# Optimization experiments

Measured on AMD Instinct MI355X. Metric: run time of the kernel, lower is better.

## Reference

```python
import jax, jax.numpy as jnp
import numpy as np

N = 8000      # nodes
E = 64000     # edges
F = 2560      # in_channels
H = 8         # heads
C = 320       # out_channels per head
G = 16        # graphs in batch
SLOPE = 0.2   # GATv2 default negative_slope


def setup_inputs() -> dict:
    key = jax.random.key(0)
    ks = jax.random.split(key, 20)
    inp = {
        'x': jax.random.normal(ks[0], (N, F), jnp.float32),
        'edge_index': jax.random.randint(ks[1], (2, E), 0, N, dtype=jnp.int64),
        'edge_attr': jax.random.normal(ks[2], (E, 1), jnp.float32),
        'batch': jnp.sort(jax.random.randint(ks[3], (N,), 0, G, dtype=jnp.int64)),
    }
    s_in = 1.0 / np.sqrt(F).astype(np.float32)
    s_att = 1.0 / np.sqrt(C).astype(np.float32)
    k = 4
    for layer in (1, 2):
        inp[f'Wl{layer}'] = jax.random.normal(ks[k + 0], (F, H * C), jnp.float32) * s_in
        inp[f'bl{layer}'] = jnp.zeros((H * C,), jnp.float32)
        inp[f'Wr{layer}'] = jax.random.normal(ks[k + 1], (F, H * C), jnp.float32) * s_in
        inp[f'br{layer}'] = jnp.zeros((H * C,), jnp.float32)
        inp[f'We{layer}'] = jax.random.normal(ks[k + 2], (1, H * C), jnp.float32)
        inp[f'att{layer}'] = jax.random.normal(ks[k + 3], (H, C), jnp.float32) * s_att
        inp[f'bias{layer}'] = jnp.zeros((H * C,), jnp.float32)
        k += 4
    return inp


def gatv2_layer(x, src, dst, edge_attr, Wl, bl, Wr, br, We, att, bias):
    # x: [N,F] -> out: [N, H*C]
    xl = (x @ Wl + bl).reshape(N, H, C)   # source transform (aggregated)
    xr = (x @ Wr + br).reshape(N, H, C)   # target transform
    ee = (edge_attr @ We).reshape(E, H, C)
    m = jax.nn.leaky_relu(xl[src] + xr[dst] + ee, SLOPE)  # [E,H,C]
    score = jnp.einsum('ehc,hc->eh', m, att)               # [E,H]
    # segment softmax over incoming edges of each target node
    smax = jax.ops.segment_max(score, dst, num_segments=N)  # [N,H]
    ex = jnp.exp(score - smax[dst])
    denom = jax.ops.segment_sum(ex, dst, num_segments=N)    # [N,H]
    alpha = ex / denom[dst]                                  # [E,H]
    out = jax.ops.segment_sum(xl[src] * alpha[:, :, None], dst, num_segments=N)
    return out.reshape(N, H * C) + bias


def reference(x, edge_index, edge_attr, batch,
              Wl1, bl1, Wr1, br1, We1, att1, bias1,
              Wl2, bl2, Wr2, br2, We2, att2, bias2):
    src, dst = edge_index[0], edge_index[1]
    h = gatv2_layer(x, src, dst, edge_attr, Wl1, bl1, Wr1, br1, We1, att1, bias1)
    # dropout is identity in eval mode
    h = gatv2_layer(h, src, dst, edge_attr, Wl2, bl2, Wr2, br2, We2, att2, bias2)
    # global mean pool over graphs
    sums = jax.ops.segment_sum(h, batch, num_segments=G)                 # [G, H*C]
    cnt = jax.ops.segment_sum(jnp.ones((N, 1), h.dtype), batch, num_segments=G)
    return sums / jnp.maximum(cnt, 1.0)
```

## Files before the change

### kernel.cpp

```cpp
#include <hip/hip_runtime.h>

typedef unsigned short u16;
typedef _Float16 f16;
typedef _Float16 f16x8 __attribute__((ext_vector_type(8)));
typedef _Float16 f16x2 __attribute__((ext_vector_type(2)));
typedef float f32x4 __attribute__((ext_vector_type(4)));

#define AS1 __attribute__((address_space(1)))
#define AS3 __attribute__((address_space(3)))

constexpr int N_NODES = 8000;
constexpr int N_EDGES = 64000;
constexpr int F_IN    = 2560;
constexpr int HEADS   = 8;
constexpr int CPH     = 320;
constexpr int HC      = 2560;
constexpr int NW      = 5120;
constexpr int NGRAPH  = 16;
constexpr float SLOPE = 0.2f;

__global__ __launch_bounds__(256)
void cvt_f32_f16(const float* __restrict__ in, f16* __restrict__ out, int n)
{
  const int i = (blockIdx.x * 256 + threadIdx.x) * 4;
  if (i >= n) return;
  const float4 v = *(const float4*)(in + i);
  f16 o[4] = {(f16)v.x, (f16)v.y, (f16)v.z, (f16)v.w};
  *(ushort4*)(out + i) = *(const ushort4*)o;
}

__global__ __launch_bounds__(256)
void transpose_w(const float* __restrict__ in, f16* __restrict__ out)
{
  __shared__ u16 tile[64][66];
  const int bx = blockIdx.x * 64;
  const int by = blockIdx.y * 64;
  const int tx = threadIdx.x & 63;
  const int ty = threadIdx.x >> 6;
  #pragma unroll
  for (int i = ty; i < 64; i += 4) {
    f16 h = (f16)in[(size_t)(by + i) * HC + bx + tx];
    u16 u; __builtin_memcpy(&u, &h, 2);
    tile[i][tx] = u;
  }
  __syncthreads();
  #pragma unroll
  for (int i = ty; i < 64; i += 4) {
    u16 u = tile[tx][i];
    f16 h; __builtin_memcpy(&h, &u, 2);
    out[(size_t)(bx + i) * F_IN + by + tx] = h;
  }
}

__global__ __launch_bounds__(512, 2)
void gemm_fused(const f16* __restrict__ A, const f16* __restrict__ BT,
                const float* __restrict__ bl, const float* __restrict__ br,
                f16* __restrict__ XL, f16* __restrict__ XR)
{
  __shared__ __align__(16) f16 sm[65536];
  f16* const sA0 = sm;
  f16* const sA1 = sm + 16384;
  f16* const sB0 = sm + 32768;
  f16* const sB1 = sm + 49152;

  const int t    = threadIdx.x;
  const int lane = t & 63;
  const int wave = t >> 6;

  int bid = (int)blockIdx.x;
  bid = (bid & 7) * 80 + (bid >> 3);
  const int m0 = (bid & 31) * 256;
  const int n0 = (bid >> 5) * 256;

  const int fm = (wave >> 2) * 128;
  const int fn = (wave & 3) * 64;
  const int ml = lane & 15;
  const int lq = lane >> 4;

  auto stageA = [&](f16* D, int half, int kt) {
    const int k0 = kt * 64;
    #pragma unroll
    for (int jj = 0; jj < 2; ++jj) {
      const int s  = jj * 512 + t;
      const int r  = s >> 3;
      const int lc = (s & 7) ^ (r & 7);
      int gr = m0 + half * 128 + r;
      gr = (gr < N_NODES) ? gr : (N_NODES - 1);
      const f16* g = A + (size_t)gr * F_IN + k0 + lc * 8;
      __builtin_amdgcn_global_load_lds((AS1 const void*)g,
                                       (AS3 void*)(D + half * 8192 + s * 8), 16, 0, 0);
    }
  };
  auto stageB = [&](f16* D, int half, int kt) {
    const int k0 = kt * 64;
    #pragma unroll
    for (int jj = 0; jj < 2; ++jj) {
      const int s  = jj * 512 + t;
      const int r  = s >> 3;
      const int lc = (s & 7) ^ (r & 7);
      const f16* g = BT + (size_t)(n0 + half * 128 + r) * F_IN + k0 + lc * 8;
      __builtin_amdgcn_global_load_lds((AS1 const void*)g,
                                       (AS3 void*)(D + half * 8192 + s * 8), 16, 0, 0);
    }
  };
  auto ldA = [&](const f16* S, int i, int kk) -> f16x8 {
    const int row = fm + i * 16 + ml;
    const int p   = (kk * 4 + lq) ^ (row & 7);
    return *(const f16x8*)(S + row * 64 + p * 8);
  };
  auto ldB = [&](const f16* S, int j, int kk) -> f16x8 {
    const int row = fn + j * 16 + ml;
    const int p   = (kk * 4 + lq) ^ (row & 7);
    return *(const f16x8*)(S + row * 64 + p * 8);
  };

  f32x4 acc[8][4] = {};
  f16x8 bf[4][2];

#define MMROW(i, A0_, A1_)                                                                   \
    _Pragma("unroll")                                                                        \
    for (int j = 0; j < 4; ++j) {                                                            \
      acc[i][j] = __builtin_amdgcn_mfma_f32_16x16x32_f16(A0_, bf[j][0], acc[i][j], 0, 0, 0); \
      acc[i][j] = __builtin_amdgcn_mfma_f32_16x16x32_f16(A1_, bf[j][1], acc[i][j], 0, 0, 0); \
    }

#define PHASE(SA, q, STG)                          \
  {                                                \
    const f16x8 p00 = ldA(SA, 2*(q),     0);       \
    const f16x8 p01 = ldA(SA, 2*(q),     1);       \
    const f16x8 p10 = ldA(SA, 2*(q) + 1, 0);       \
    const f16x8 p11 = ldA(SA, 2*(q) + 1, 1);       \
    STG;                                           \
    __builtin_amdgcn_s_barrier();                  \
    __builtin_amdgcn_sched_barrier(0);             \
    __builtin_amdgcn_s_setprio(1);                 \
    MMROW(2*(q),     p00, p01)                     \
    MMROW(2*(q) + 1, p10, p11)                     \
    __builtin_amdgcn_s_setprio(0);                 \
  }

#define ENDPH() { __builtin_amdgcn_s_barrier(); __builtin_amdgcn_sched_barrier(0); }
#define LOADB(SB) { _Pragma("unroll") for (int j = 0; j < 4; ++j) { bf[j][0] = ldB(SB, j, 0); bf[j][1] = ldB(SB, j, 1); } }

  stageA(sA0, 0, 0); stageA(sA0, 1, 0);
  stageB(sB0, 0, 0); stageB(sB0, 1, 0);
  stageB(sB1, 0, 1); stageB(sB1, 1, 1);
  asm volatile("s_waitcnt vmcnt(4)" ::: "memory");
  __builtin_amdgcn_s_barrier();
  __builtin_amdgcn_sched_barrier(0);

  for (int it = 0; it < 20; ++it) {
    const int T  = 2 * it;
    const int t1 = T + 1;
    const int t2 = (T + 2 < 40) ? T + 2 : 39;
    const int t3 = (T + 3 < 40) ? T + 3 : 39;

    LOADB(sB0)
    PHASE(sA0, 0, stageA(sA1, 0, t1)) ENDPH()
    PHASE(sA0, 1, stageA(sA1, 1, t1)) ENDPH()
    PHASE(sA0, 2, stageB(sB0, 0, t2)) ENDPH()
    PHASE(sA0, 3, stageB(sB0, 1, t2))
    asm volatile("s_waitcnt vmcnt(4)" ::: "memory");
    ENDPH()
    LOADB(sB1)
    PHASE(sA1, 0, stageA(sA0, 0, t2)) ENDPH()
    PHASE(sA1, 1, stageA(sA0, 1, t2)) ENDPH()
    PHASE(sA1, 2, stageB(sB1, 0, t3)) ENDPH()
    PHASE(sA1, 3, stageB(sB1, 1, t3))
    asm volatile("s_waitcnt vmcnt(4)" ::: "memory");
    ENDPH()
  }

#undef MMROW
#undef PHASE
#undef ENDPH
#undef LOADB

  const bool left = (n0 < HC);
  f16* __restrict__ OUT = left ? XL : XR;
  const float* __restrict__ bias = left ? bl : br;
  const int nb = left ? n0 : (n0 - HC);
  const int rg = (lane >> 4) * 4;
  #pragma unroll
  for (int j = 0; j < 4; ++j) {
    const int gn = nb + fn + j * 16 + ml;
    const float bv = bias[gn];
    #pragma unroll
    for (int i = 0; i < 8; ++i) {
      #pragma unroll
      for (int r = 0; r < 4; ++r) {
        const int gm = m0 + fm + i * 16 + rg + r;
        if (gm < N_NODES) OUT[(size_t)gm * HC + gn] = (f16)(acc[i][j][r] + bv);
      }
    }
  }
}

__global__ __launch_bounds__(256)
void count_edges(const int* __restrict__ dst, int* __restrict__ counts)
{
  const int e = blockIdx.x * 256 + threadIdx.x;
  if (e < N_EDGES) atomicAdd(&counts[dst[e]], 1);
}

__global__ __launch_bounds__(256)
void scan_offsets(const int* __restrict__ counts, int* __restrict__ offs, int* __restrict__ cur)
{
  __shared__ int wtot[4];
  const int t = threadIdx.x;
  const int lane = t & 63, wave = t >> 6;
  const int base = t * 32;
  int loc[32];
  int run = 0;
  #pragma unroll
  for (int i = 0; i < 32; ++i) {
    const int idx = base + i;
    const int v = (idx < N_NODES) ? counts[idx] : 0;
    loc[i] = run;
    run += v;
  }
  int incl = run;
  #pragma unroll
  for (int off = 1; off < 64; off <<= 1) {
    int y = __shfl_up(incl, off, 64);
    if (lane >= off) incl += y;
  }
  const int excl = incl - run;
  if (lane == 63) wtot[wave] = incl;
  __syncthreads();
  int wb = 0;
  for (int wv = 0; wv < wave; ++wv) wb += wtot[wv];
  const int mybase = wb + excl;
  #pragma unroll
  for (int i = 0; i < 32; ++i) {
    const int idx = base + i;
    if (idx < N_NODES) { offs[idx] = mybase + loc[i]; cur[idx] = mybase + loc[i]; }
  }
  if (t == 255) offs[N_NODES] = wb + incl;
}

__global__ __launch_bounds__(256)
void fill_csr(const int* __restrict__ dst, int* __restrict__ cur, int* __restrict__ eids)
{
  const int e = blockIdx.x * 256 + threadIdx.x;
  if (e < N_EDGES) {
    const int p = atomicAdd(&cur[dst[e]], 1);
    eids[p] = e;
  }
}

__global__ __launch_bounds__(256)
void gat_edge_fused(const f16* __restrict__ XL, const f16* __restrict__ XR,
                    const float* __restrict__ We, const float* __restrict__ att,
                    const float* __restrict__ eattr,
                    const int* __restrict__ src,
                    const int* __restrict__ offs, const int* __restrict__ eids,
                    const float* __restrict__ bias,
                    f16* __restrict__ out)
{
  const int n    = blockIdx.x;
  const int t    = threadIdx.x;
  const int wave = t >> 6;
  const int lane = t & 63;
  const int half = lane >> 5;
  const int l32  = lane & 31;
  const int h    = wave * 2 + half;
  const int c8   = h * CPH + l32 * 8;
  const int c2   = h * CPH + 256 + l32 * 2;

  float xr[10], wv[10], av[10];
  {
    const f16x8 v8 = *(const f16x8*)(XR + (size_t)n * HC + c8);
    const f16x2 v2 = *(const f16x2*)(XR + (size_t)n * HC + c2);
    #pragma unroll
    for (int k = 0; k < 8; ++k) xr[k] = (float)v8[k];
    xr[8] = (float)v2[0]; xr[9] = (float)v2[1];
  }
  {
    const float4 w0 = *(const float4*)(We + c8);
    const float4 w1 = *(const float4*)(We + c8 + 4);
    const float4 a0 = *(const float4*)(att + c8);
    const float4 a1 = *(const float4*)(att + c8 + 4);
    wv[0]=w0.x; wv[1]=w0.y; wv[2]=w0.z; wv[3]=w0.w;
    wv[4]=w1.x; wv[5]=w1.y; wv[6]=w1.z; wv[7]=w1.w;
    av[0]=a0.x; av[1]=a0.y; av[2]=a0.z; av[3]=a0.w;
    av[4]=a1.x; av[5]=a1.y; av[6]=a1.z; av[7]=a1.w;
    wv[8] = We[c2]; wv[9] = We[c2 + 1];
    av[8] = att[c2]; av[9] = att[c2 + 1];
  }

  float m = -3.0e38f, l = 0.f;
  float acc[10];
  #pragma unroll
  for (int k = 0; k < 10; ++k) acc[k] = 0.f;

  const int b = offs[n], e = offs[n + 1];
  for (int p = b; p < e; ++p) {
    const int eid  = eids[p];
    const int s    = src[eid];
    const float ea = eattr[eid];
    const f16* row = XL + (size_t)s * HC;
    const f16x8 v8 = *(const f16x8*)(row + c8);
    const f16x2 v2 = *(const f16x2*)(row + c2);
    float xl[10];
    #pragma unroll
    for (int k = 0; k < 8; ++k) xl[k] = (float)v8[k];
    xl[8] = (float)v2[0]; xl[9] = (float)v2[1];
    float partial = 0.f;
    #pragma unroll
    for (int k = 0; k < 10; ++k) {
      float v = xl[k] + xr[k] + ea * wv[k];
      v = (v > 0.f) ? v : SLOPE * v;
      partial += v * av[k];
    }
    #pragma unroll
    for (int msk = 16; msk >= 1; msk >>= 1)
      partial += __shfl_xor(partial, msk, 64);
    const float sc    = partial;
    const float mn    = fmaxf(m, sc);
    const float scale = __expf(m - mn);
    const float w     = __expf(sc - mn);
    l = l * scale + w;
    #pragma unroll
    for (int k = 0; k < 10; ++k) acc[k] = acc[k] * scale + w * xl[k];
    m = mn;
  }

  const float inv = (l > 0.f) ? 1.f / l : 0.f;
  f16x8 s8;
  #pragma unroll
  for (int k = 0; k < 8; ++k) s8[k] = (f16)(acc[k] * inv + bias[c8 + k]);
  f16x2 s2;
  s2[0] = (f16)(acc[8] * inv + bias[c2]);
  s2[1] = (f16)(acc[9] * inv + bias[c2 + 1]);
  *(f16x8*)(out + (size_t)n * HC + c8) = s8;
  *(f16x2*)(out + (size_t)n * HC + c2) = s2;
}

__global__ __launch_bounds__(256)
void pool_kernel(const f16* __restrict__ Hm, const int* __restrict__ batch, float* __restrict__ out)
{
  __shared__ int se[2];
  const int g = blockIdx.x;
  const int chunk = blockIdx.y;
  const int t = threadIdx.x;
  if (t < 2) {
    const int target = g + t;
    int lo = 0, hi = N_NODES;
    while (lo < hi) { const int mid = (lo + hi) >> 1; if (batch[mid] < target) lo = mid + 1; else hi = mid; }
    se[t] = lo;
  }
  __syncthreads();
  const int s0 = se[0], s1 = se[1];
  const int c = chunk * 256 + t;
  float sum = 0.f;
  for (int n = s0; n < s1; ++n) sum += (float)Hm[(size_t)n * HC + c];
  int cnt = s1 - s0; if (cnt < 1) cnt = 1;
  out[g * HC + c] = sum / (float)cnt;
}

static void run_layer(const f16* A, const float* Wl, const float* bl,
                      const float* Wr, const float* br,
                      const float* We, const float* att, const float* bias,
                      const int* src, const float* eattr,
                      f16* WT, f16* XL, f16* XR,
                      const int* offs, const int* eids, f16* OUT, hipStream_t stream)
{
  dim3 tgrid(HC / 64, F_IN / 64);
  transpose_w<<<tgrid, 256, 0, stream>>>(Wl, WT);
  transpose_w<<<tgrid, 256, 0, stream>>>(Wr, WT + (size_t)HC * F_IN);
  gemm_fused<<<32 * (NW / 256), 512, 0, stream>>>(A, WT, bl, br, XL, XR);
  gat_edge_fused<<<N_NODES, 256, 0, stream>>>(XL, XR, We, att, eattr, src, offs, eids, bias, OUT);
}

extern "C" void kernel_launch(void* const* d_in, const int* in_sizes, int n_in,
                              void* d_out, int out_size, void* d_ws, size_t ws_size,
                              hipStream_t stream)
{
  const float* x     = (const float*)d_in[0];
  const int*   eidx  = (const int*)d_in[1];
  const float* eattr = (const float*)d_in[2];
  const int*   batch = (const int*)d_in[3];
  const float* Wl1  = (const float*)d_in[4];
  const float* bl1  = (const float*)d_in[5];
  const float* Wr1  = (const float*)d_in[6];
  const float* br1  = (const float*)d_in[7];
  const float* We1  = (const float*)d_in[8];
  const float* att1 = (const float*)d_in[9];
  const float* bias1= (const float*)d_in[10];
  const float* Wl2  = (const float*)d_in[11];
  const float* bl2  = (const float*)d_in[12];
  const float* Wr2  = (const float*)d_in[13];
  const float* br2  = (const float*)d_in[14];
  const float* We2  = (const float*)d_in[15];
  const float* att2 = (const float*)d_in[16];
  const float* bias2= (const float*)d_in[17];
  float* out = (float*)d_out;

  const int* src = eidx;
  const int* dst = eidx + N_EDGES;

  char* w = (char*)d_ws;
  auto take = [&](size_t b) { char* p = w; w += (b + 255) & ~(size_t)255; return p; };
  f16*   Xh    = (f16*)take((size_t)N_NODES * F_IN * 2);
  f16*   H2h   = (f16*)take((size_t)N_NODES * HC * 2);
  f16*   WT    = (f16*)take((size_t)NW * F_IN * 2);
  f16*   XL    = (f16*)take((size_t)N_NODES * HC * 2);
  f16*   XR    = (f16*)take((size_t)N_NODES * HC * 2);
  int*   counts= (int*)take((size_t)N_NODES * 4);
  int*   offs  = (int*)take((size_t)(N_NODES + 1) * 4);
  int*   cur   = (int*)take((size_t)N_NODES * 4);
  int*   eids  = (int*)take((size_t)N_EDGES * 4);

  hipMemsetAsync(counts, 0, N_NODES * 4, stream);
  count_edges<<<N_EDGES / 256, 256, 0, stream>>>(dst, counts);
  scan_offsets<<<1, 256, 0, stream>>>(counts, offs, cur);
  fill_csr<<<N_EDGES / 256, 256, 0, stream>>>(dst, cur, eids);

  cvt_f32_f16<<<(N_NODES * F_IN) / 1024, 256, 0, stream>>>(x, Xh, N_NODES * F_IN);

  run_layer(Xh, Wl1, bl1, Wr1, br1, We1, att1, bias1, src, eattr,
            WT, XL, XR, offs, eids, Xh, stream);
  run_layer(Xh, Wl2, bl2, Wr2, br2, We2, att2, bias2, src, eattr,
            WT, XL, XR, offs, eids, H2h, stream);

  pool_kernel<<<dim3(NGRAPH, HC / 256), 256, 0, stream>>>(H2h, batch, out);
}
```

Baseline: 1.010 ms.

## Stage GEMM epilogue through LDS, remap XCD tiles, prefetch edge gathers

The GEMM epilogue now writes each wave's accumulator tile into swizzled shared memory and then stores 16-byte vectors per row to global, replacing scattered 2-byte stores. The block-to-tile mapping is changed so each XCD gets a contiguous band of M rows, aiming for better L2 reuse of A. The edge aggregation loop is software-pipelined, loading the next source row and the edge index two steps ahead to hide gather latency. The cost is an extra barrier and LDS round trip in the epilogue, plus more registers in the aggregation loop.

```diff
diff --git a/kernel.cpp b/kernel.cpp
--- a/kernel.cpp
+++ b/kernel.cpp
@@ -67,10 +67,11 @@
   const int lane = t & 63;
   const int wave = t >> 6;
 
-  int bid = (int)blockIdx.x;
-  bid = (bid & 7) * 80 + (bid >> 3);
-  const int m0 = (bid & 31) * 256;
-  const int n0 = (bid >> 5) * 256;
+  const int bid0 = (int)blockIdx.x;
+  const int xcd  = bid0 & 7;
+  const int ic   = bid0 >> 3;
+  const int m0   = (xcd * 4 + (ic & 3)) * 256;
+  const int n0   = (ic >> 2) * 256;
 
   const int fm = (wave >> 2) * 128;
   const int fn = (wave & 3) * 64;
@@ -176,23 +177,40 @@
 #undef ENDPH
 #undef LOADB
 
+  asm volatile("s_waitcnt vmcnt(0)" ::: "memory");
+  __builtin_amdgcn_s_barrier();
+
   const bool left = (n0 < HC);
   f16* __restrict__ OUT = left ? XL : XR;
   const float* __restrict__ bias = left ? bl : br;
   const int nb = left ? n0 : (n0 - HC);
   const int rg = (lane >> 4) * 4;
+  f16* const wbase = sm + wave * 8192;
+
   #pragma unroll
   for (int j = 0; j < 4; ++j) {
-    const int gn = nb + fn + j * 16 + ml;
-    const float bv = bias[gn];
+    const float bv = bias[nb + fn + j * 16 + ml];
     #pragma unroll
     for (int i = 0; i < 8; ++i) {
       #pragma unroll
       for (int r = 0; r < 4; ++r) {
-        const int gm = m0 + fm + i * 16 + rg + r;
-        if (gm < N_NODES) OUT[(size_t)gm * HC + gn] = (f16)(acc[i][j][r] + bv);
+        const int row = i * 16 + rg + r;
+        const int col = j * 16 + ml;
+        const int pc  = (col >> 3) ^ (row & 7);
+        wbase[row * 64 + pc * 8 + (col & 7)] = (f16)(acc[i][j][r] + bv);
       }
     }
+  }
+  __syncthreads();
+  #pragma unroll
+  for (int it = 0; it < 16; ++it) {
+    const int row = it * 8 + (lane >> 3);
+    const int ch  = lane & 7;
+    const int pc  = ch ^ (row & 7);
+    const f16x8 v = *(const f16x8*)(wbase + row * 64 + pc * 8);
+    const int gm = m0 + fm + row;
+    if (gm < N_NODES)
+      *(f16x8*)(OUT + (size_t)gm * HC + nb + fn + ch * 8) = v;
   }
 }
 
@@ -295,35 +313,51 @@
   for (int k = 0; k < 10; ++k) acc[k] = 0.f;
 
   const int b = offs[n], e = offs[n + 1];
-  for (int p = b; p < e; ++p) {
-    const int eid  = eids[p];
-    const int s    = src[eid];
-    const float ea = eattr[eid];
-    const f16* row = XL + (size_t)s * HC;
-    const f16x8 v8 = *(const f16x8*)(row + c8);
-    const f16x2 v2 = *(const f16x2*)(row + c2);
-    float xl[10];
-    #pragma unroll
-    for (int k = 0; k < 8; ++k) xl[k] = (float)v8[k];
-    xl[8] = (float)v2[0]; xl[9] = (float)v2[1];
-    float partial = 0.f;
-    #pragma unroll
-    for (int k = 0; k < 10; ++k) {
-      float v = xl[k] + xr[k] + ea * wv[k];
-      v = (v > 0.f) ? v : SLOPE * v;
-      partial += v * av[k];
+  if (b < e) {
+    int eidA = eids[b];
+    int sA   = src[eidA];
+    float eaA = eattr[eidA];
+    f16x8 v8A = *(const f16x8*)(XL + (size_t)sA * HC + c8);
+    f16x2 v2A = *(const f16x2*)(XL + (size_t)sA * HC + c2);
+    int sB; float eaB;
+    if (b + 1 < e) { const int eid = eids[b + 1]; sB = src[eid]; eaB = eattr[eid]; }
+    else           { sB = sA; eaB = 0.f; }
+
+    for (int p = b; p < e; ++p) {
+      const f16* rowN = XL + (size_t)sB * HC;
+      const f16x8 v8N = *(const f16x8*)(rowN + c8);
+      const f16x2 v2N = *(const f16x2*)(rowN + c2);
+      const int pn   = (p + 2 < e) ? (p + 2) : (e - 1);
+      const int eidN = eids[pn];
+      const int sC   = src[eidN];
+      const float eaC = eattr[eidN];
+
+      float xl[10];
+      #pragma unroll
+      for (int k = 0; k < 8; ++k) xl[k] = (float)v8A[k];
+      xl[8] = (float)v2A[0]; xl[9] = (float)v2A[1];
+      float partial = 0.f;
+      #pragma unroll
+      for (int k = 0; k < 10; ++k) {
+        float v = xl[k] + xr[k] + eaA * wv[k];
+        v = (v > 0.f) ? v : SLOPE * v;
+        partial += v * av[k];
+      }
+      #pragma unroll
+      for (int msk = 16; msk >= 1; msk >>= 1)
+        partial += __shfl_xor(partial, msk, 64);
+      const float sc    = partial;
+      const float mn    = fmaxf(m, sc);
+      const float scale = __expf(m - mn);
+      const float w     = __expf(sc - mn);
+      l = l * scale + w;
+      #pragma unroll
+      for (int k = 0; k < 10; ++k) acc[k] = acc[k] * scale + w * xl[k];
+      m = mn;
+
+      v8A = v8N; v2A = v2N; eaA = eaB;
+      sB = sC; eaB = eaC;
     }
-    #pragma unroll
-    for (int msk = 16; msk >= 1; msk >>= 1)
-      partial += __shfl_xor(partial, msk, 64);
-    const float sc    = partial;
-    const float mn    = fmaxf(m, sc);
-    const float scale = __expf(m - mn);
-    const float w     = __expf(sc - mn);
-    l = l * scale + w;
-    #pragma unroll
-    for (int k = 0; k < 10; ++k) acc[k] = acc[k] * scale + w * xl[k];
-    m = mn;
   }
 
   const float inv = (l > 0.f) ? 1.f / l : 0.f;
```

Result: faster. 915.4 us (-9.4%).
